# Performance work log

Hardware: AMD Instinct MI355X
Metric: run time of the kernel (lower is better)

Reference implementation:

```python
import jax, jax.numpy as jnp
import numpy as np

NUM_CLASSES = 8
NUM_MAPS = 4
FEAT_C = 2048  # ResNet-50 layer4 channels
HW = 14        # spatial size (448/32)


def setup_inputs() -> dict:
    key = jax.random.key(0)
    k1, k2, k3, k4, k5 = jax.random.split(key, 5)
    B = 64
    x = jax.random.normal(k1, (B, FEAT_C, HW, HW), dtype=jnp.float32)
    down_w = jax.random.normal(k2, (NUM_CLASSES * NUM_MAPS, FEAT_C), dtype=jnp.float32) * 0.02
    down_b = jax.random.normal(k3, (NUM_CLASSES * NUM_MAPS,), dtype=jnp.float32) * 0.02
    fc_w = jax.random.normal(k4, (NUM_CLASSES, 2 * FEAT_C), dtype=jnp.float32) * 0.02
    fc_b = jax.random.normal(k5, (NUM_CLASSES,), dtype=jnp.float32) * 0.02
    return {"x": x, "down_w": down_w, "down_b": down_b, "fc_w": fc_w, "fc_b": fc_b}


def reference(x, down_w, down_b, fc_w, fc_b):
    B = x.shape[0]
    x_ori = x  # [B, 2048, 14, 14] (ResNet features output)
    # downconv: 1x1 conv 2048 -> num_classes*num_maps
    xc = jnp.einsum('bchw,oc->bohw', x_ori, down_w) + down_b[None, :, None, None]  # [B,32,14,14]
    # GMP over full 14x14 window -> [B, 32]
    gmp = jnp.max(xc, axis=(2, 3))
    # spatial_pooling = ClassWisePool(num_maps): mean over groups of num_maps channels
    scores = gmp.reshape(B, NUM_CLASSES, NUM_MAPS).mean(axis=2)  # [B, 8]
    x_out = jax.nn.log_softmax(scores, axis=1)  # first output
    # class-wise pool on the full conv map: [B,32,14,14] -> [B,8,14,14]
    xcp = xc.reshape(B, NUM_CLASSES, NUM_MAPS, HW, HW).mean(axis=2)
    # modulate each class map by its (log-softmax) score
    xcp = xcp * x_out[:, :, None, None]
    # spatial_pooling2 = ClassWisePool(num_classes): mean over 8 class channels -> [B,1,14,14]
    sal = xcp.mean(axis=1, keepdims=True)
    prod = sal * x_ori  # [B,2048,14,14] via broadcast (fused, no copies)
    cat = jnp.concatenate([x_ori, prod], axis=1)  # [B,4096,14,14]
    # GAP 14x14 -> [B,4096]
    gap = cat.mean(axis=(2, 3))
    logits2 = gap @ fc_w.T + fc_b  # [B,8]
    x_conv_out = jax.nn.log_softmax(logits2, axis=1)
    return (x_out, x_conv_out)
```

## Files before the change

kernel.cpp:

```cpp
#include <hip/hip_runtime.h>

#define NCH 2048
#define HW 196
#define NB 64
#define NOUT 48
#define NCHUNK 16
#define CPC (NCH / NCHUNK)
#define KSTEPS (CPC / 32)
#define KGTOT (NCH / 32)
#define NT 13
#define MT 3

typedef __attribute__((ext_vector_type(8))) short bf16x8;
typedef __attribute__((ext_vector_type(4))) float f32x4;

__device__ __forceinline__ short f2bf(float f) {
    unsigned int u = __float_as_uint(f);
    u = u + 0x7fffu + ((u >> 16) & 1u);
    return (short)(u >> 16);
}

__global__ void build_afrag(const float* __restrict__ down_w,
                            const float* __restrict__ fc_w,
                            bf16x8* __restrict__ afrag) {
    int t = blockIdx.x * 256 + threadIdx.x;
    if (t >= KGTOT * MT * 64) return;
    int lane = t & 63;
    int frag = t >> 6;
    int mt = frag % MT;
    int kg = frag / MT;
    int o = mt * 16 + (lane & 15);
    int cbase = kg * 32 + (lane >> 4) * 8;
    bf16x8 v;
#pragma unroll
    for (int j = 0; j < 8; ++j) {
        int c = cbase + j;
        float w;
        if (o < 32)      w = down_w[o * NCH + c];
        else if (o < 40) w = fc_w[(o - 32) * (2 * NCH) + NCH + c];
        else             w = fc_w[(o - 40) * (2 * NCH) + c];
        v[j] = f2bf(w);
    }
    afrag[frag * 64 + lane] = v;
}

__global__ __launch_bounds__(256, 4) void conv_mfma(const float* __restrict__ x,
                                                    const bf16x8* __restrict__ afrag,
                                                    float* __restrict__ part) {
    const int chunk = blockIdx.x;
    const int b = blockIdx.y;
    const int wave = threadIdx.x >> 6;
    const int lane = threadIdx.x & 63;
    const int nsub = lane & 15;
    const int kq = lane >> 4;

    f32x4 acc[4][MT];
#pragma unroll
    for (int i = 0; i < 4; ++i)
#pragma unroll
        for (int m = 0; m < MT; ++m)
            acc[i][m] = (f32x4){0.f, 0.f, 0.f, 0.f};

    int pidx[4];
#pragma unroll
    for (int i = 0; i < 4; ++i) {
        int p = (wave + 4 * i) * 16 + nsub;
        pidx[i] = (p < HW) ? p : (HW - 1);
    }

    const float* xb = x + ((size_t)b * NCH + (size_t)chunk * CPC) * HW;

    for (int ks = 0; ks < KSTEPS; ++ks) {
        const int kg = chunk * KSTEPS + ks;
        bf16x8 a0 = afrag[(kg * MT + 0) * 64 + lane];
        bf16x8 a1 = afrag[(kg * MT + 1) * 64 + lane];
        bf16x8 a2 = afrag[(kg * MT + 2) * 64 + lane];
        const float* xk = xb + (ks * 32 + kq * 8) * HW;
#pragma unroll
        for (int i = 0; i < 4; ++i) {
            float f[8];
#pragma unroll
            for (int j = 0; j < 8; ++j) f[j] = xk[j * HW + pidx[i]];
            bf16x8 bv;
#pragma unroll
            for (int j = 0; j < 8; ++j) bv[j] = f2bf(f[j]);
            acc[i][0] = __builtin_amdgcn_mfma_f32_16x16x32_bf16(a0, bv, acc[i][0], 0, 0, 0);
            acc[i][1] = __builtin_amdgcn_mfma_f32_16x16x32_bf16(a1, bv, acc[i][1], 0, 0, 0);
            acc[i][2] = __builtin_amdgcn_mfma_f32_16x16x32_bf16(a2, bv, acc[i][2], 0, 0, 0);
        }
    }

    float* dst = part + ((size_t)(b * NCHUNK + chunk) * NOUT) * HW;
#pragma unroll
    for (int i = 0; i < 4; ++i) {
        int nt = wave + 4 * i;
        int p = nt * 16 + nsub;
        if (nt < NT && p < HW) {
#pragma unroll
            for (int m = 0; m < MT; ++m)
#pragma unroll
                for (int r = 0; r < 4; ++r)
                    dst[(m * 16 + kq * 4 + r) * HW + p] = acc[i][m][r];
        }
    }
}

__global__ __launch_bounds__(256) void reduce_part(const float* __restrict__ part,
                                                   float* __restrict__ T) {
    int idx = blockIdx.x * 256 + threadIdx.x;
    if (idx >= NB * NOUT * HW) return;
    int b = idx / (NOUT * HW);
    int rem = idx - b * (NOUT * HW);
    const float* src = part + (size_t)b * NCHUNK * NOUT * HW + rem;
    float s = 0.f;
#pragma unroll
    for (int ch = 0; ch < NCHUNK; ++ch)
        s += src[(size_t)ch * NOUT * HW];
    T[idx] = s;
}

__global__ __launch_bounds__(256) void finish(const float* __restrict__ T,
                                              const float* __restrict__ down_b,
                                              const float* __restrict__ fc_b,
                                              float* __restrict__ out) {
    const int b = blockIdx.x;
    const int tid = threadIdx.x;
    __shared__ float Ts[NOUT * HW];
    __shared__ float gmpS[32];
    __shared__ float scoreS[8];
    __shared__ float xoS[8];
    __shared__ float salS[HW];
    __shared__ float logitS[8];

    {
        const float4* src = (const float4*)(T + (size_t)b * NOUT * HW);
        float4* dst = (float4*)Ts;
        for (int i = tid; i < NOUT * HW / 4; i += 256) dst[i] = src[i];
    }
    __syncthreads();

    if (tid < 32) {
        float m = -1e30f;
        for (int p = 0; p < HW; ++p) m = fmaxf(m, Ts[tid * HW + p]);
        gmpS[tid] = m + down_b[tid];
    }
    __syncthreads();

    if (tid < 8)
        scoreS[tid] = 0.25f * (gmpS[4 * tid] + gmpS[4 * tid + 1] +
                               gmpS[4 * tid + 2] + gmpS[4 * tid + 3]);
    __syncthreads();

    if (tid < 8) {
        float m = -1e30f;
        for (int k = 0; k < 8; ++k) m = fmaxf(m, scoreS[k]);
        float se = 0.f;
        for (int k = 0; k < 8; ++k) se += expf(scoreS[k] - m);
        float xo = scoreS[tid] - m - logf(se);
        xoS[tid] = xo;
        out[b * 8 + tid] = xo;
    }
    __syncthreads();

    if (tid < HW) {
        float s = 0.f;
#pragma unroll
        for (int k = 0; k < 8; ++k) {
            float bs = down_b[4 * k] + down_b[4 * k + 1] +
                       down_b[4 * k + 2] + down_b[4 * k + 3];
            float rs = Ts[(4 * k) * HW + tid] + Ts[(4 * k + 1) * HW + tid] +
                       Ts[(4 * k + 2) * HW + tid] + Ts[(4 * k + 3) * HW + tid] + bs;
            s += xoS[k] * rs;
        }
        salS[tid] = s * (1.f / 32.f);
    }
    __syncthreads();

    if (tid < 8) {
        float t1 = 0.f, t2 = 0.f;
        for (int p = 0; p < HW; ++p) {
            t1 += Ts[(40 + tid) * HW + p];
            t2 += salS[p] * Ts[(32 + tid) * HW + p];
        }
        logitS[tid] = (t1 + t2) * (1.f / 196.f) + fc_b[tid];
    }
    __syncthreads();

    if (tid < 8) {
        float m = -1e30f;
        for (int k = 0; k < 8; ++k) m = fmaxf(m, logitS[k]);
        float se = 0.f;
        for (int k = 0; k < 8; ++k) se += expf(logitS[k] - m);
        out[NB * 8 + b * 8 + tid] = logitS[tid] - m - logf(se);
    }
}

extern "C" void kernel_launch(void* const* d_in, const int* in_sizes, int n_in,
                              void* d_out, int out_size, void* d_ws, size_t ws_size,
                              hipStream_t stream) {
    const float* x      = (const float*)d_in[0];
    const float* down_w = (const float*)d_in[1];
    const float* down_b = (const float*)d_in[2];
    const float* fc_w   = (const float*)d_in[3];
    const float* fc_b   = (const float*)d_in[4];
    float* out = (float*)d_out;

    bf16x8* afrag = (bf16x8*)d_ws;
    float* T    = (float*)((char*)d_ws + (size_t)KGTOT * MT * 64 * 16);
    float* part = T + (size_t)NB * NOUT * HW;

    build_afrag<<<(KGTOT * MT * 64 + 255) / 256, 256, 0, stream>>>(down_w, fc_w, afrag);
    conv_mfma<<<dim3(NCHUNK, NB), 256, 0, stream>>>(x, afrag, part);
    reduce_part<<<(NB * NOUT * HW + 255) / 256, 256, 0, stream>>>(part, T);
    finish<<<NB, 256, 0, stream>>>(T, down_b, fc_b, out);
}
```

Baseline: 202.0 us.

## Stage x tiles into LDS with double-buffered async global_load_lds

```diff
diff --git a/kernel.cpp b/kernel.cpp
--- a/kernel.cpp
+++ b/kernel.cpp
@@ -4,12 +4,14 @@
 #define HW 196
 #define NB 64
 #define NOUT 48
-#define NCHUNK 16
+#define NCHUNK 8
 #define CPC (NCH / NCHUNK)
-#define KSTEPS (CPC / 32)
+#define KS_PER_BLK (CPC / 32)
 #define KGTOT (NCH / 32)
 #define NT 13
 #define MT 3
+#define TILE_F (32 * HW)
+#define TILE_V4 (TILE_F / 4)
 
 typedef __attribute__((ext_vector_type(8))) short bf16x8;
 typedef __attribute__((ext_vector_type(4))) float f32x4;
@@ -44,13 +46,15 @@
     afrag[frag * 64 + lane] = v;
 }
 
-__global__ __launch_bounds__(256, 4) void conv_mfma(const float* __restrict__ x,
-                                                    const bf16x8* __restrict__ afrag,
-                                                    float* __restrict__ part) {
+__global__ __launch_bounds__(256) void conv_mfma(const float* __restrict__ x,
+                                                 const bf16x8* __restrict__ afrag,
+                                                 float* __restrict__ part) {
+    __shared__ float ldsx[2][TILE_F];
     const int chunk = blockIdx.x;
     const int b = blockIdx.y;
-    const int wave = threadIdx.x >> 6;
-    const int lane = threadIdx.x & 63;
+    const int tid = threadIdx.x;
+    const int wave = tid >> 6;
+    const int lane = tid & 63;
     const int nsub = lane & 15;
     const int kq = lane >> 4;
 
@@ -68,19 +72,40 @@
         pidx[i] = (p < HW) ? p : (HW - 1);
     }
 
-    const float* xb = x + ((size_t)b * NCH + (size_t)chunk * CPC) * HW;
-
-    for (int ks = 0; ks < KSTEPS; ++ks) {
-        const int kg = chunk * KSTEPS + ks;
+    const float* xtile0 = x + ((size_t)b * NCH + (size_t)chunk * CPC) * HW;
+
+    auto stage = [&](int ks, int bb) {
+        const float* g = xtile0 + (size_t)ks * TILE_F;
+#pragma unroll
+        for (int r = 0; r < 7; ++r) {
+            int q = r * 256 + tid;
+            if (q < TILE_V4) {
+                __builtin_amdgcn_global_load_lds(
+                    (const __attribute__((address_space(1))) unsigned int*)(g + (size_t)q * 4),
+                    (__attribute__((address_space(3))) unsigned int*)(&ldsx[bb][(r * 256 + wave * 64) * 4]),
+                    16, 0, 0);
+            }
+        }
+    };
+
+    stage(0, 0);
+
+    for (int ks = 0; ks < KS_PER_BLK; ++ks) {
+        __syncthreads();
+        if (ks + 1 < KS_PER_BLK) stage(ks + 1, (ks + 1) & 1);
+
+        const int kg = chunk * KS_PER_BLK + ks;
         bf16x8 a0 = afrag[(kg * MT + 0) * 64 + lane];
         bf16x8 a1 = afrag[(kg * MT + 1) * 64 + lane];
         bf16x8 a2 = afrag[(kg * MT + 2) * 64 + lane];
-        const float* xk = xb + (ks * 32 + kq * 8) * HW;
+
+        const float* base = &ldsx[ks & 1][kq * 8 * HW];
 #pragma unroll
         for (int i = 0; i < 4; ++i) {
+            const float* bp = base + pidx[i];
             float f[8];
 #pragma unroll
-            for (int j = 0; j < 8; ++j) f[j] = xk[j * HW + pidx[i]];
+            for (int j = 0; j < 8; ++j) f[j] = bp[j * HW];
             bf16x8 bv;
 #pragma unroll
             for (int j = 0; j < 8; ++j) bv[j] = f2bf(f[j]);
@@ -90,17 +115,17 @@
         }
     }
 
-    float* dst = part + ((size_t)(b * NCHUNK + chunk) * NOUT) * HW;
+    float* pb = part + (size_t)(b * NCHUNK + chunk) * (NT * NOUT * 16);
 #pragma unroll
     for (int i = 0; i < 4; ++i) {
         int nt = wave + 4 * i;
-        int p = nt * 16 + nsub;
-        if (nt < NT && p < HW) {
+        if (nt < NT) {
+            float* d = pb + nt * (NOUT * 16) + kq * 64 + nsub;
 #pragma unroll
             for (int m = 0; m < MT; ++m)
 #pragma unroll
                 for (int r = 0; r < 4; ++r)
-                    dst[(m * 16 + kq * 4 + r) * HW + p] = acc[i][m][r];
+                    d[m * 256 + r * 16] = acc[i][m][r];
         }
     }
 }
@@ -111,11 +136,15 @@
     if (idx >= NB * NOUT * HW) return;
     int b = idx / (NOUT * HW);
     int rem = idx - b * (NOUT * HW);
-    const float* src = part + (size_t)b * NCHUNK * NOUT * HW + rem;
+    int o = rem / HW;
+    int p = rem - o * HW;
+    int nt = p >> 4, ns = p & 15;
+    const float* src = part + (size_t)b * NCHUNK * NT * NOUT * 16
+                     + nt * (NOUT * 16) + o * 16 + ns;
     float s = 0.f;
 #pragma unroll
     for (int ch = 0; ch < NCHUNK; ++ch)
-        s += src[(size_t)ch * NOUT * HW];
+        s += src[(size_t)ch * NT * NOUT * 16];
     T[idx] = s;
 }
 
```

Result: faster. 186.2 us (-7.8%).
